# Kernel optimization log

Hardware: AMD Instinct MI355X
Metric: run time of the kernel (lower is better)

Reference implementation:

```python
import jax, jax.numpy as jnp
import numpy as np

NH = 12   # heads
KD = 64   # key_dim = dim // heads


def setup_inputs() -> dict:
    key = jax.random.key(0)
    ks = jax.random.split(key, 6)
    B, N, C = 64, 1024, 768
    qkv_out = (1 + 2 * KD) * NH  # 1548
    s = 0.02
    return {
        "x": jax.random.normal(ks[0], (B, N, C), dtype=jnp.float32),
        "w_qkv": jax.random.normal(ks[1], (qkv_out, C), dtype=jnp.float32) * s,
        "b_qkv": jax.random.normal(ks[2], (qkv_out,), dtype=jnp.float32) * s,
        "w_cv": jax.random.normal(ks[3], (1, N), dtype=jnp.float32) * s,
        "w_out": jax.random.normal(ks[4], (C, C), dtype=jnp.float32) * s,
        "b_out": jax.random.normal(ks[5], (C,), dtype=jnp.float32) * s,
    }


def reference(x, w_qkv, b_qkv, w_cv, w_out, b_out):
    B, N, C = x.shape
    # qkv projection: [B, N, (1+2*KD)*NH] -> [B, N, NH, 1+2*KD]
    qkv = (jnp.einsum("bnc,oc->bno", x, w_qkv) + b_qkv).reshape(B, N, NH, 1 + 2 * KD)
    q = qkv[..., :1]                 # [B, N, NH, 1]
    k = qkv[..., 1:1 + KD]           # [B, N, NH, KD]
    v = qkv[..., 1 + KD:]            # [B, N, NH, KD]
    # softmax pooling over the token axis N (dropout p=0 -> identity)
    scores = jax.nn.softmax(q, axis=1)          # [B, N, NH, 1]
    # cv_proj: Linear(token_len -> 1), no bias, applied over token axis
    cv = jnp.einsum("bnhd,n->bhd", k * scores, w_cv[0])  # [B, NH, KD]
    # gated ReLU: relu(value) * broadcast context vector
    out = jax.nn.relu(v) * cv[:, None, :, :]    # [B, N, NH, KD]
    out = out.reshape(B, N, NH * KD)
    return jnp.einsum("bnc,oc->bno", out, w_out) + b_out
```

## Files before the change

### kernel.cpp

```cpp
#include <hip/hip_runtime.h>
#include <hip/hip_bf16.h>

typedef unsigned short u16;
typedef __attribute__((ext_vector_type(8))) short bf16x8;
typedef __attribute__((ext_vector_type(8))) unsigned short u16x8;
typedef __attribute__((ext_vector_type(4))) float f32x4;

#define NHh 12
#define KDd 64
#define Bb 64
#define Nn 1024
#define Cc 768
#define Oo 1548
#define Mm 65536

__device__ __forceinline__ float bf2f(u16 u) {
    union { unsigned int i; float f; } x; x.i = ((unsigned int)u) << 16; return x.f;
}
__device__ __forceinline__ u16 f2bf(float f) {
    union { float f; unsigned int i; } x; x.f = f;
    unsigned int r = x.i + 0x7fffu + ((x.i >> 16) & 1u);
    return (u16)(r >> 16);
}
__device__ __forceinline__ unsigned int cvtpk(float a, float b) {
    unsigned int r;
    asm("v_cvt_pk_bf16_f32 %0, %1, %2" : "=v"(r) : "v"(a), "v"(b));
    return r;
}

__device__ __forceinline__ void async16(const u16* g, u16* l) {
    __builtin_amdgcn_global_load_lds(
        (const __attribute__((address_space(1))) void*)g,
        (__attribute__((address_space(3))) void*)l, 16, 0, 0);
}

__global__ void detect_kernel(const u16* __restrict__ w, int* __restrict__ flag)
{
    __shared__ int cnt;
    if (threadIdx.x == 0) cnt = 0;
    __syncthreads();
    int c = 0;
#pragma unroll
    for (int i = 0; i < 4; ++i) {
        const u16 u = w[(threadIdx.x * 4 + i) * 2];
        const int e = (u >> 7) & 0xFF;
        c += ((e >= 0x60 && e <= 0x9F) || u == 0) ? 1 : 0;
    }
    atomicAdd(&cnt, c);
    __syncthreads();
    if (threadIdx.x == 0) flag[0] = (cnt >= 160) ? 1 : 0;
}

__global__ __launch_bounds__(256) void cvt_kernel(
    const float* __restrict__ src, u16* __restrict__ dst, int n16,
    const int* __restrict__ flagp)
{
    if (flagp[0]) return;
    const int i = blockIdx.x * 256 + threadIdx.x;
    if (i >= n16) return;
    const float* p = src + (size_t)i * 16;
    const f32x4 a0 = *(const f32x4*)p;
    const f32x4 a1 = *(const f32x4*)(p + 4);
    const f32x4 a2 = *(const f32x4*)(p + 8);
    const f32x4 a3 = *(const f32x4*)(p + 12);
    union { unsigned int u[8]; u16x8 v[2]; } pk;
    pk.u[0] = cvtpk(a0[0], a0[1]); pk.u[1] = cvtpk(a0[2], a0[3]);
    pk.u[2] = cvtpk(a1[0], a1[1]); pk.u[3] = cvtpk(a1[2], a1[3]);
    pk.u[4] = cvtpk(a2[0], a2[1]); pk.u[5] = cvtpk(a2[2], a2[3]);
    pk.u[6] = cvtpk(a3[0], a3[1]); pk.u[7] = cvtpk(a3[2], a3[3]);
    *(u16x8*)(dst + (size_t)i * 16)     = pk.v[0];
    *(u16x8*)(dst + (size_t)i * 16 + 8) = pk.v[1];
}

template <int EPI>
__global__ __launch_bounds__(256, 4) void gemm_bt(
    const void* __restrict__ Aorig, const u16* __restrict__ Acvt,
    const void* __restrict__ Borig, const u16* __restrict__ Bcvt,
    const void* __restrict__ biasv, const int* __restrict__ flagp,
    int Nout, int K, int lda, int ldb, int ntn,
    float* __restrict__ Qf, u16* __restrict__ Kb, u16* __restrict__ Vb,
    u16* __restrict__ Cout16, float* __restrict__ Cout32, int ldc)
{
    __shared__ __align__(16) u16 lA[128 * 64];
    __shared__ __align__(16) u16 lB[128 * 64];

    const int isbf = flagp[0];
    const u16* A  = isbf ? (const u16*)Aorig : Acvt;
    const u16* Bp = isbf ? (const u16*)Borig : Bcvt;

    const int t = threadIdx.x;
    const int lane = t & 63, wave = t >> 6;

    int bid = blockIdx.x;
    {
        const int nwg = (int)gridDim.x;
        const int cpx = nwg >> 3;
        bid = (bid & 7) * cpx + (bid >> 3);
    }
    const int tm = bid / ntn, tn = bid % ntn;
    const int m0 = tm * 128, o0 = tn * 128;

    const int srow = t >> 3;
    const int scol = (t & 7) * 8;
    const int ssw  = (((t & 7) ^ (srow & 7)) * 8);

    const int R0 = (wave >> 1) * 64, C0 = (wave & 1) * 64;
    const int lr = lane & 15, lq = lane >> 4;
    const int sw8 = lr & 7;

    const u16* aSrc[4];
    const u16* bSrc[4];
#pragma unroll
    for (int i = 0; i < 4; ++i) {
        aSrc[i] = A + (size_t)(m0 + i * 32 + srow) * lda + ssw;
        int o = o0 + i * 32 + srow;
        if (o > Nout - 1) o = Nout - 1;
        bSrc[i] = Bp + (size_t)o * ldb + ssw;
    }

    f32x4 acc[4][4];
    const f32x4 zero = {0.f, 0.f, 0.f, 0.f};
#pragma unroll
    for (int i = 0; i < 4; ++i)
#pragma unroll
        for (int j = 0; j < 4; ++j) acc[i][j] = zero;

    for (int k0 = 0; k0 < K; k0 += 64) {
#pragma unroll
        for (int i = 0; i < 4; ++i)
            async16(aSrc[i] + k0, &lA[(i * 32 + srow) * 64 + scol]);
#pragma unroll
        for (int i = 0; i < 4; ++i)
            async16(bSrc[i] + k0, &lB[(i * 32 + srow) * 64 + scol]);

        asm volatile("s_waitcnt vmcnt(0)" ::: "memory");
        __syncthreads();

#pragma unroll
        for (int kk = 0; kk < 2; ++kk) {
            bf16x8 af[4], bfr[4];
            const int sl = (((kk * 4 + lq) ^ sw8) * 8);
#pragma unroll
            for (int i = 0; i < 4; ++i)
                af[i] = *(const bf16x8*)&lA[(R0 + i * 16 + lr) * 64 + sl];
#pragma unroll
            for (int j = 0; j < 4; ++j)
                bfr[j] = *(const bf16x8*)&lB[(C0 + j * 16 + lr) * 64 + sl];
#pragma unroll
            for (int i = 0; i < 4; ++i)
#pragma unroll
                for (int j = 0; j < 4; ++j)
                    acc[i][j] = __builtin_amdgcn_mfma_f32_16x16x32_bf16(af[i], bfr[j], acc[i][j], 0, 0, 0);
        }
        __syncthreads();
    }

#pragma unroll
    for (int i = 0; i < 4; ++i) {
#pragma unroll
        for (int j = 0; j < 4; ++j) {
            const int ob = o0 + C0 + j * 16 + lr;
            float bv = 0.f;
            if (ob < Nout)
                bv = isbf ? bf2f(((const u16*)biasv)[ob]) : ((const float*)biasv)[ob];
#pragma unroll
            for (int r = 0; r < 4; ++r) {
                const int row = m0 + R0 + i * 16 + lq * 4 + r;
                const float val = acc[i][j][r] + bv;
                if (EPI == 1) {
                    if (ob < Nout) {
                        const int h = ob / 129;
                        const int rr = ob - h * 129;
                        const size_t mh = (size_t)row * 12 + h;
                        if (rr == 0)       Qf[mh] = val;
                        else if (rr <= 64) Kb[mh * 64 + (rr - 1)]  = f2bf(val);
                        else               Vb[mh * 64 + (rr - 65)] = f2bf(val);
                    }
                } else {
                    if (isbf) Cout16[(size_t)row * ldc + ob] = f2bf(val);
                    else      Cout32[(size_t)row * ldc + ob] = val;
                }
            }
        }
    }
}

__global__ __launch_bounds__(256) void softmax_cv_kernel(
    const float* __restrict__ Qf, const u16* __restrict__ Kb,
    const void* __restrict__ wcvv, const int* __restrict__ flagp,
    float* __restrict__ cv)
{
    const int isbf = flagp[0];
    const int bh = blockIdx.x;
    const int b = bh / NHh, h = bh - (bh / NHh) * NHh;
    const int t = threadIdx.x;

    __shared__ float sp[1024];
    __shared__ float red[256];

    float q[4];
#pragma unroll
    for (int i = 0; i < 4; ++i) {
        const int n = t + i * 256;
        q[i] = Qf[(size_t)(b * Nn + n) * NHh + h];
    }
    float mx = fmaxf(fmaxf(q[0], q[1]), fmaxf(q[2], q[3]));
    red[t] = mx; __syncthreads();
    for (int off = 128; off; off >>= 1) {
        if (t < off) red[t] = fmaxf(red[t], red[t + off]);
        __syncthreads();
    }
    mx = red[0];
    __syncthreads();

    float sloc = 0.f;
#pragma unroll
    for (int i = 0; i < 4; ++i) {
        const int n = t + i * 256;
        const float e = __expf(q[i] - mx);
        sloc += e;
        const float wv = isbf ? bf2f(((const u16*)wcvv)[n]) : ((const float*)wcvv)[n];
        sp[n] = e * wv;
    }
    red[t] = sloc; __syncthreads();
    for (int off = 128; off; off >>= 1) {
        if (t < off) red[t] += red[t + off];
        __syncthreads();
    }
    const float s = red[0];
    __syncthreads();

    const int d = t & 63, g = t >> 6;
    const u16* Kp = Kb + ((size_t)(b * Nn + g * 256) * NHh + h) * 64 + d;
    const float* pp = sp + g * 256;
    float acc = 0.f;
#pragma unroll 8
    for (int n = 0; n < 256; ++n)
        acc = fmaf(bf2f(Kp[(size_t)n * 768]), pp[n], acc);

    red[t] = acc; __syncthreads();
    if (t < 64) {
        const float tot = red[t] + red[t + 64] + red[t + 128] + red[t + 192];
        cv[(size_t)bh * 64 + t] = tot / s;
    }
}

__global__ __launch_bounds__(256) void relu_cv_kernel(
    u16* __restrict__ Vb, const float* __restrict__ cv)
{
    const size_t idx = ((size_t)blockIdx.x * 256 + threadIdx.x) * 8;
    const int c = (int)(idx % 768);
    const size_t m = idx / 768;
    const int b = (int)(m >> 10);
    const int h = c >> 6, d0 = c & 63;
    const float* cvp = cv + ((size_t)b * NHh + h) * 64 + d0;

    u16x8 r = *(const u16x8*)(Vb + idx);
#pragma unroll
    for (int i = 0; i < 8; ++i) {
        const float f = fmaxf(bf2f(r[i]), 0.f) * cvp[i];
        r[i] = f2bf(f);
    }
    *(u16x8*)(Vb + idx) = r;
}

extern "C" void kernel_launch(void* const* d_in, const int* in_sizes, int n_in,
                              void* d_out, int out_size, void* d_ws, size_t ws_size,
                              hipStream_t stream)
{
    const void* x     = d_in[0];
    const void* w_qkv = d_in[1];
    const void* b_qkv = d_in[2];
    const void* w_cv  = d_in[3];
    const void* w_out = d_in[4];
    const void* b_out = d_in[5];

    char* w = (char*)d_ws;
    float* Qf = (float*)w;
    u16*   Kb = (u16*)(w + 3145728);
    u16*   Vb = (u16*)(w + 3145728 + 100663296);
    float* cv = (float*)(w + 3145728 + 2ll * 100663296);
    int* flag = (int*)(w + 3145728 + 2ll * 100663296 + 196608);
    u16* wqkvb = (u16*)(w + 3145728 + 2ll * 100663296 + 196608 + 4096);
    u16* woutb = (u16*)((char*)wqkvb + 2377728);

    u16* xb = (u16*)d_out;

    detect_kernel<<<1, 64, 0, stream>>>((const u16*)w_qkv, flag);

    cvt_kernel<<<(Mm * Cc) / (256 * 16), 256, 0, stream>>>((const float*)x, xb, (Mm * Cc) / 16, flag);
    cvt_kernel<<<(Oo * Cc + 256 * 16 - 1) / (256 * 16), 256, 0, stream>>>((const float*)w_qkv, wqkvb, (Oo * Cc) / 16, flag);
    cvt_kernel<<<(Cc * Cc) / (256 * 16), 256, 0, stream>>>((const float*)w_out, woutb, (Cc * Cc) / 16, flag);

    gemm_bt<1><<<512 * 13, 256, 0, stream>>>(x, xb, w_qkv, wqkvb, b_qkv, flag,
        Oo, Cc, Cc, Cc, 13, Qf, Kb, Vb, nullptr, nullptr, 0);

    softmax_cv_kernel<<<Bb * NHh, 256, 0, stream>>>(Qf, Kb, w_cv, flag, cv);

    relu_cv_kernel<<<(Mm * 768) / (256 * 8), 256, 0, stream>>>(Vb, cv);

    gemm_bt<2><<<512 * 6, 256, 0, stream>>>(Vb, (const u16*)Vb, w_out, woutb, b_out, flag,
        Cc, Cc, Cc, Cc, 6, nullptr, nullptr, nullptr, (u16*)d_out, (float*)d_out, Cc);
}
```

Baseline: 751.1 us.

## Double-buffer GEMM LDS tiles with 256x128 blocks and vectorize cv reduction

The GEMM now uses 512-thread blocks covering 256x128 output tiles with two LDS buffers, so the next K-slice is loaded asynchronously while MFMAs run on the current one, with setprio and sched_barrier hints. This is meant to hide global-load latency and halve B-tile reloads per output row. The softmax-cv kernel switches to 16-byte vector loads of K with a padded shared-memory transpose reduction instead of strided scalar loads. LDS use grows to 96KB per block, which limits occupancy, and the single barrier per iteration relies on the vmcnt wait for correctness.

```diff
diff --git a/kernel.cpp b/kernel.cpp
--- a/kernel.cpp
+++ b/kernel.cpp
@@ -73,7 +73,7 @@
 }
 
 template <int EPI>
-__global__ __launch_bounds__(256, 4) void gemm_bt(
+__global__ __launch_bounds__(512, 2) void gemm_bt(
     const void* __restrict__ Aorig, const u16* __restrict__ Acvt,
     const void* __restrict__ Borig, const u16* __restrict__ Bcvt,
     const void* __restrict__ biasv, const int* __restrict__ flagp,
@@ -81,8 +81,8 @@
     float* __restrict__ Qf, u16* __restrict__ Kb, u16* __restrict__ Vb,
     u16* __restrict__ Cout16, float* __restrict__ Cout32, int ldc)
 {
-    __shared__ __align__(16) u16 lA[128 * 64];
-    __shared__ __align__(16) u16 lB[128 * 64];
+    __shared__ __align__(16) u16 lA2[2 * 256 * 64];
+    __shared__ __align__(16) u16 lB2[2 * 128 * 64];
 
     const int isbf = flagp[0];
     const u16* A  = isbf ? (const u16*)Aorig : Acvt;
@@ -98,22 +98,25 @@
         bid = (bid & 7) * cpx + (bid >> 3);
     }
     const int tm = bid / ntn, tn = bid % ntn;
-    const int m0 = tm * 128, o0 = tn * 128;
+    const int m0 = tm * 256, o0 = tn * 128;
 
     const int srow = t >> 3;
     const int scol = (t & 7) * 8;
     const int ssw  = (((t & 7) ^ (srow & 7)) * 8);
 
-    const int R0 = (wave >> 1) * 64, C0 = (wave & 1) * 64;
+    const int wr = wave >> 1, wc = wave & 1;
+    const int R0 = wr * 64, C0 = wc * 64;
     const int lr = lane & 15, lq = lane >> 4;
     const int sw8 = lr & 7;
 
     const u16* aSrc[4];
-    const u16* bSrc[4];
-#pragma unroll
-    for (int i = 0; i < 4; ++i) {
-        aSrc[i] = A + (size_t)(m0 + i * 32 + srow) * lda + ssw;
-        int o = o0 + i * 32 + srow;
+    const u16* bSrc[2];
+#pragma unroll
+    for (int i = 0; i < 4; ++i)
+        aSrc[i] = A + (size_t)(m0 + i * 64 + srow) * lda + ssw;
+#pragma unroll
+    for (int i = 0; i < 2; ++i) {
+        int o = o0 + i * 64 + srow;
         if (o > Nout - 1) o = Nout - 1;
         bSrc[i] = Bp + (size_t)o * ldb + ssw;
     }
@@ -125,34 +128,52 @@
 #pragma unroll
         for (int j = 0; j < 4; ++j) acc[i][j] = zero;
 
-    for (int k0 = 0; k0 < K; k0 += 64) {
+    auto STAGE = [&](int kt, int buf) {
+        const int k0 = kt * 64;
+        u16* la = &lA2[buf * (256 * 64)];
+        u16* lb = &lB2[buf * (128 * 64)];
 #pragma unroll
         for (int i = 0; i < 4; ++i)
-            async16(aSrc[i] + k0, &lA[(i * 32 + srow) * 64 + scol]);
-#pragma unroll
-        for (int i = 0; i < 4; ++i)
-            async16(bSrc[i] + k0, &lB[(i * 32 + srow) * 64 + scol]);
-
-        asm volatile("s_waitcnt vmcnt(0)" ::: "memory");
-        __syncthreads();
-
+            async16(aSrc[i] + k0, &la[(i * 64 + srow) * 64 + scol]);
+#pragma unroll
+        for (int i = 0; i < 2; ++i)
+            async16(bSrc[i] + k0, &lb[(i * 64 + srow) * 64 + scol]);
+    };
+
+    const int NT = K >> 6;
+    STAGE(0, 0);
+    asm volatile("s_waitcnt vmcnt(0)" ::: "memory");
+    __builtin_amdgcn_s_barrier();
+    __builtin_amdgcn_sched_barrier(0);
+
+    for (int kt = 0; kt < NT; ++kt) {
+        const int cur = kt & 1;
+        if (kt + 1 < NT) STAGE(kt + 1, cur ^ 1);
+        __builtin_amdgcn_sched_barrier(0);
+
+        const u16* la = &lA2[cur * (256 * 64)];
+        const u16* lb = &lB2[cur * (128 * 64)];
+        __builtin_amdgcn_s_setprio(1);
 #pragma unroll
         for (int kk = 0; kk < 2; ++kk) {
             bf16x8 af[4], bfr[4];
             const int sl = (((kk * 4 + lq) ^ sw8) * 8);
 #pragma unroll
             for (int i = 0; i < 4; ++i)
-                af[i] = *(const bf16x8*)&lA[(R0 + i * 16 + lr) * 64 + sl];
+                af[i] = *(const bf16x8*)&la[(R0 + i * 16 + lr) * 64 + sl];
 #pragma unroll
             for (int j = 0; j < 4; ++j)
-                bfr[j] = *(const bf16x8*)&lB[(C0 + j * 16 + lr) * 64 + sl];
+                bfr[j] = *(const bf16x8*)&lb[(C0 + j * 16 + lr) * 64 + sl];
 #pragma unroll
             for (int i = 0; i < 4; ++i)
 #pragma unroll
                 for (int j = 0; j < 4; ++j)
                     acc[i][j] = __builtin_amdgcn_mfma_f32_16x16x32_bf16(af[i], bfr[j], acc[i][j], 0, 0, 0);
         }
-        __syncthreads();
+        __builtin_amdgcn_s_setprio(0);
+        __builtin_amdgcn_sched_barrier(0);
+        asm volatile("s_waitcnt vmcnt(0)" ::: "memory");
+        __builtin_amdgcn_s_barrier();
     }
 
 #pragma unroll
@@ -197,6 +218,7 @@
 
     __shared__ float sp[1024];
     __shared__ float red[256];
+    __shared__ float redd[64 * 33];
 
     float q[4];
 #pragma unroll
@@ -230,17 +252,27 @@
     const float s = red[0];
     __syncthreads();
 
-    const int d = t & 63, g = t >> 6;
-    const u16* Kp = Kb + ((size_t)(b * Nn + g * 256) * NHh + h) * 64 + d;
-    const float* pp = sp + g * 256;
-    float acc = 0.f;
+    const int dt8 = (t & 7) * 8;
+    const int ng  = t >> 3;
+    float a8[8];
+#pragma unroll
+    for (int i = 0; i < 8; ++i) a8[i] = 0.f;
+    const u16* Kbase = Kb + ((size_t)b * Nn * NHh + h) * 64 + dt8;
+#pragma unroll 4
+    for (int it = 0; it < 32; ++it) {
+        const int n = it * 32 + ng;
+        const u16x8 kv = *(const u16x8*)(Kbase + (size_t)n * 768);
+        const float p = sp[n];
+#pragma unroll
+        for (int i = 0; i < 8; ++i) a8[i] = fmaf(bf2f(kv[i]), p, a8[i]);
+    }
+#pragma unroll
+    for (int i = 0; i < 8; ++i) redd[(dt8 + i) * 33 + ng] = a8[i];
+    __syncthreads();
+    if (t < 64) {
+        float tot = 0.f;
 #pragma unroll 8
-    for (int n = 0; n < 256; ++n)
-        acc = fmaf(bf2f(Kp[(size_t)n * 768]), pp[n], acc);
-
-    red[t] = acc; __syncthreads();
-    if (t < 64) {
-        const float tot = red[t] + red[t + 64] + red[t + 128] + red[t + 192];
+        for (int g2 = 0; g2 < 32; ++g2) tot += redd[t * 33 + g2];
         cv[(size_t)bh * 64 + t] = tot / s;
     }
 }
@@ -292,13 +324,13 @@
     cvt_kernel<<<(Oo * Cc + 256 * 16 - 1) / (256 * 16), 256, 0, stream>>>((const float*)w_qkv, wqkvb, (Oo * Cc) / 16, flag);
     cvt_kernel<<<(Cc * Cc) / (256 * 16), 256, 0, stream>>>((const float*)w_out, woutb, (Cc * Cc) / 16, flag);
 
-    gemm_bt<1><<<512 * 13, 256, 0, stream>>>(x, xb, w_qkv, wqkvb, b_qkv, flag,
+    gemm_bt<1><<<256 * 13, 512, 0, stream>>>(x, xb, w_qkv, wqkvb, b_qkv, flag,
         Oo, Cc, Cc, Cc, 13, Qf, Kb, Vb, nullptr, nullptr, 0);
 
     softmax_cv_kernel<<<Bb * NHh, 256, 0, stream>>>(Qf, Kb, w_cv, flag, cv);
 
     relu_cv_kernel<<<(Mm * 768) / (256 * 8), 256, 0, stream>>>(Vb, cv);
 
-    gemm_bt<2><<<512 * 6, 256, 0, stream>>>(Vb, (const u16*)Vb, w_out, woutb, b_out, flag,
+    gemm_bt<2><<<256 * 6, 512, 0, stream>>>(Vb, (const u16*)Vb, w_out, woutb, b_out, flag,
         Cc, Cc, Cc, Cc, 6, nullptr, nullptr, nullptr, (u16*)d_out, (float*)d_out, Cc);
 }
```

After: 899.6 us. 19.8% more time.
